# Kernel tuning notes

Hardware: AMD Instinct MI355X
Metric: run time of the kernel (lower is better)

The kernel has to match this reference:

```python
import jax, jax.numpy as jnp
import numpy as np
from jax import lax

N, T, U, V = 32, 512, 100, 4096
BLANK = 0


def setup_inputs() -> dict:
    key = jax.random.key(0)
    k1, k2, k3, k4, k5 = jax.random.split(key, 5)
    encoder_out = jax.random.normal(k1, (N, T, V), dtype=jnp.float32)
    decoder_out = jax.random.normal(k2, (N, U + 1, V), dtype=jnp.float32)
    targets = jax.random.randint(k3, (N, U), 1, V)            # labels, never blank
    input_lengths = jax.random.randint(k4, (N,), T // 2, T + 1)
    target_lengths = jax.random.randint(k5, (N,), U // 2, U + 1)
    return {
        "encoder_out": encoder_out,
        "decoder_out": decoder_out,
        "targets": targets,
        "input_lengths": input_lengths,
        "target_lengths": target_lengths,
    }


def _logprob_single(enc, dec, y, in_len, tgt_len):
    # enc: (T, V)  dec: (U+1, V)  y: (U,)
    Um = y.shape[0]
    u_idx = jnp.arange(Um)
    # emit[t, u] = enc[t, y[u]] + dec[u, y[u]]  (cost of emitting label u+1 at time t)
    emit = enc[:, y] + dec[u_idx, y][None, :]          # (T, U)
    blank_e = enc[:, BLANK]                            # (T,)
    blank_d = dec[:, BLANK]                            # (U+1,)

    # t = 0 row: alpha[0, u] = sum_{k<u} emit[0, k]
    alpha0 = jnp.concatenate([jnp.zeros((1,), enc.dtype), jnp.cumsum(emit[0])])

    def row_step(alpha_prev, xs):
        be_prev, emit_t = xs
        # blank transition from row t-1 (same u)
        top = alpha_prev + be_prev + blank_d           # (U+1,)

        # label transition within row: alpha[u] = logaddexp(top[u], alpha[u-1] + emit_t[u-1])
        def u_step(carry, x):
            top_u, em = x
            a = jnp.logaddexp(top_u, carry + em)
            return a, a

        _, rest = lax.scan(u_step, top[0], (top[1:], emit_t))
        alpha = jnp.concatenate([top[:1], rest])
        return alpha, alpha

    _, rows = lax.scan(row_step, alpha0, (blank_e[:-1], emit[1:]))
    alphas = jnp.concatenate([alpha0[None, :], rows], axis=0)   # (T, U+1)

    # log p(y|x) = alpha[T-1, U] + enc[T-1, blank] + dec[U, blank] with true lengths
    return alphas[in_len - 1, tgt_len] + enc[in_len - 1, BLANK] + dec[tgt_len, BLANK]


def reference(encoder_out, decoder_out, targets, input_lengths, target_lengths):
    # reduction='none': returns per-utterance log p(y|x), shape (N,)
    return jax.vmap(_logprob_single)(encoder_out, decoder_out, targets,
                                     input_lengths, target_lengths)
```

## Files before the change

### kernel.cpp

```cpp
#include <hip/hip_runtime.h>

#define NB 32
#define TT 512
#define UU 100
#define UM 101
#define VV 4096
#define NEG (-1e30f)
#define PW 16
#define WINB 32
#define NWIN 22
#define DST 720
#define L2E 1.4426950408889634f
#define LN2 0.6931471805599453f

__device__ __forceinline__ float vexp2(float x){ float r; asm("v_exp_f32 %0, %1" : "=v"(r) : "v"(x)); return r; }
__device__ __forceinline__ float vlog2(float x){ float r; asm("v_log_f32 %0, %1" : "=v"(r) : "v"(x)); return r; }

__device__ __forceinline__ float lae2(float a, float b) {
    float m  = fmaxf(a, b);
    float nd = fminf(a, b) - m;
    return m + vlog2(1.0f + vexp2(nd));
}

__global__ __launch_bounds__(256) void build_k(
        const float* __restrict__ enc, const float* __restrict__ dec,
        const int* __restrict__ tgt, const int* __restrict__ ilen,
        const int* __restrict__ tlen, float* __restrict__ st) {
    int w = blockIdx.x, n = blockIdx.y;
    int tid = threadIdx.x;
    __shared__ int   tgtL[UU];
    __shared__ float dvxL[UU];
    if (tid < UU) {
        int y = tgt[n * UU + tid];
        tgtL[tid] = y;
        dvxL[tid] = dec[((size_t)n * UM + tid) * VV + y] * L2E;
    }
    int tin = ilen[n], tg = tlen[n];
    __syncthreads();
    const float* encn = enc + (size_t)n * TT * VV;

    float ev[16];
#pragma unroll
    for (int it = 0; it < 16; ++it) {
        int idx = tid + it * 256;
        int dm = idx >> 7, u = idx & 127;
        int d = w * WINB + 1 + dm;
        int t = d - u;
        bool ok = (u >= 1) & (u <= tg) & (t >= 0) & (t < tin);
        ev[it] = NEG;
        if (ok) ev[it] = encn[(size_t)t * VV + tgtL[u - 1]];
    }
#pragma unroll
    for (int it = 0; it < 16; ++it) {
        int idx = tid + it * 256;
        int dm = idx >> 7, u = idx & 127;
        int d = w * WINB + 1 + dm;
        int t = d - u;
        bool ok = (u >= 1) & (u <= tg) & (t >= 0) & (t < tin);
        int uc = max(u, 1);
        float e = ok ? fmaf(ev[it], L2E, dvxL[uc - 1]) : NEG;
        st[((size_t)n * DST + d) * 128 + u] = e;
    }
}

__global__ __launch_bounds__(256) void dp_k(
        const float* __restrict__ enc, const float* __restrict__ dec,
        const int* __restrict__ ilen, const int* __restrict__ tlen,
        const float* __restrict__ st, float* __restrict__ out) {
    int n = blockIdx.x;
    int tid = threadIdx.x;
    __shared__ float blkL[864];
    const float* encn = enc + (size_t)n * TT * VV;
    for (int i = tid; i < 864; i += 256)
        blkL[i] = (i >= 128 && i < 128 + TT) ? encn[(size_t)(i - 128) * VV] * L2E : NEG;
    __syncthreads();
    if (tid >= 64) return;
    int lane = tid;

    int tin = ilen[n], tg = tlen[n];
    int dend = tin - 1 + tg;
    const float* decn = dec + (size_t)n * UM * VV;
    float bd0 = decn[(size_t)min(2 * lane, UM - 1) * VV] * L2E;
    float bd1 = decn[(size_t)min(2 * lane + 1, UM - 1) * VV] * L2E;
    const float* sp = st + (size_t)n * DST * 128 + 2 * lane;
    int ib0 = 127 - 2 * lane;
    bool cap0 = (2 * lane == tg), cap1 = (2 * lane + 1 == tg);
    bool fx16 = (lane == 16), fx32 = (lane == 32), fx48 = (lane == 48);
    float a0 = (lane == 0) ? 0.0f : NEG;
    float a1 = NEG;
    float res = NEG;

    float Ae0[PW], Ae1[PW], Ab0[PW], Ab1[PW];
    float Be0[PW], Be1[PW], Bb0[PW], Bb1[PW];

    auto REFILL = [&](float (&Re0)[PW], float (&Re1)[PW],
                      float (&Rb0)[PW], float (&Rb1)[PW], int d0) {
#pragma unroll
        for (int k = 0; k < PW; ++k) {
            int d = d0 + k;
            float2 ev = *(const float2*)(sp + (size_t)d * 128);
            Re0[k] = ev.x; Re1[k] = ev.y;
            Rb0[k] = blkL[ib0 + d] + bd0;
            Rb1[k] = blkL[ib0 + d - 1] + bd1;
        }
        __builtin_amdgcn_sched_barrier(0);
    };

    auto STEPS = [&](float (&Re0)[PW], float (&Re1)[PW],
                     float (&Rb0)[PW], float (&Rb1)[PW], int d0) {
#pragma unroll
        for (int k = 0; k < PW; ++k) {
            int dd = d0 + k;
            int sh = __builtin_amdgcn_update_dpp(__float_as_int(NEG), __float_as_int(a1),
                                                 0x111, 0xF, 0xF, false);
            float s15 = __int_as_float(__builtin_amdgcn_readlane(__float_as_int(a1), 15));
            float s31 = __int_as_float(__builtin_amdgcn_readlane(__float_as_int(a1), 31));
            float s47 = __int_as_float(__builtin_amdgcn_readlane(__float_as_int(a1), 47));
            float l0 = __int_as_float(sh);
            l0 = fx16 ? s15 : l0;
            l0 = fx32 ? s31 : l0;
            l0 = fx48 ? s47 : l0;
            float bt0 = a0 + Rb0[k], et0 = l0 + Re0[k];
            float bt1 = a1 + Rb1[k], et1 = a0 + Re1[k];
            a0 = lae2(bt0, et0);
            a1 = lae2(bt1, et1);
            if (dd == dend) { if (cap0) res = a0; if (cap1) res = a1; }
        }
        __builtin_amdgcn_sched_barrier(0);
    };

    REFILL(Ae0, Ae1, Ab0, Ab1, 1);
    for (int d0 = 1; d0 <= dend; d0 += 2 * PW) {
        REFILL(Be0, Be1, Bb0, Bb1, d0 + PW);     STEPS(Ae0, Ae1, Ab0, Ab1, d0);
        REFILL(Ae0, Ae1, Ab0, Ab1, d0 + 2 * PW); STEPS(Be0, Be1, Bb0, Bb1, d0 + PW);
    }

    if (cap0 | cap1) {
        float fin  = blkL[128 + tin - 1];
        float bdtg = decn[(size_t)tg * VV] * L2E;
        out[n] = (res + fin + bdtg) * LN2;
    }
}

extern "C" void kernel_launch(void* const* d_in, const int* in_sizes, int n_in,
                              void* d_out, int out_size, void* d_ws, size_t ws_size,
                              hipStream_t hs) {
    const float* enc  = (const float*)d_in[0];
    const float* dec  = (const float*)d_in[1];
    const int*   tgt  = (const int*)d_in[2];
    const int*   ilen = (const int*)d_in[3];
    const int*   tlen = (const int*)d_in[4];
    float* out = (float*)d_out;
    float* st  = (float*)d_ws;

    hipLaunchKernelGGL(build_k, dim3(NWIN, NB), dim3(256), 0, hs,
                       enc, dec, tgt, ilen, tlen, st);
    hipLaunchKernelGGL(dp_k, dim3(NB), dim3(256), 0, hs,
                       enc, dec, ilen, tlen, st, out);
}
```

Measured before the change: 73.29 us.

## Fuse gather and DP kernels with per-window flags to overlap producer and consumer

Merges the emission-gather kernel and the diagonal DP kernel into one launch. Producer blocks fill diagonal windows and publish per-window ready flags, while the DP blocks spin on those flags before each refill, so the wavefront recurrence can start before the whole staging buffer is written. It also drops windows past each utterance's length and uses fewer producer blocks that loop over windows. The cost is an extra flag-clear launch, spin-wait latency, and relying on producer blocks being scheduled alongside the spinning consumers.

```diff
diff --git a/kernel.cpp b/kernel.cpp
--- a/kernel.cpp
+++ b/kernel.cpp
@@ -8,7 +8,8 @@
 #define NEG (-1e30f)
 #define PW 16
 #define WINB 32
-#define NWIN 22
+#define NWIN 20
+#define GSTRIDE 5
 #define DST 720
 #define L2E 1.4426950408889634f
 #define LN2 0.6931471805599453f
@@ -22,53 +23,68 @@
     return m + vlog2(1.0f + vexp2(nd));
 }
 
-__global__ __launch_bounds__(256) void build_k(
+__global__ void clear_k(int* __restrict__ flags) {
+    flags[threadIdx.x] = 0;
+}
+
+__global__ __launch_bounds__(256, 1) void fused_k(
         const float* __restrict__ enc, const float* __restrict__ dec,
         const int* __restrict__ tgt, const int* __restrict__ ilen,
-        const int* __restrict__ tlen, float* __restrict__ st) {
-    int w = blockIdx.x, n = blockIdx.y;
+        const int* __restrict__ tlen,
+        float* __restrict__ st, int* __restrict__ flags, float* __restrict__ out) {
+    int bid = blockIdx.x;
     int tid = threadIdx.x;
-    __shared__ int   tgtL[UU];
-    __shared__ float dvxL[UU];
-    if (tid < UU) {
-        int y = tgt[n * UU + tid];
-        tgtL[tid] = y;
-        dvxL[tid] = dec[((size_t)n * UM + tid) * VV + y] * L2E;
+
+    if (bid >= NB) {
+        int pb = bid - NB;
+        int n = pb / GSTRIDE, g = pb % GSTRIDE;
+        __shared__ int   tgtL[UU];
+        __shared__ float dvxL[UU];
+        if (tid < UU) {
+            int y = tgt[n * UU + tid];
+            tgtL[tid] = y;
+            dvxL[tid] = dec[((size_t)n * UM + tid) * VV + y] * L2E;
+        }
+        int tin = ilen[n], tg = tlen[n];
+        __syncthreads();
+        const float* encn = enc + (size_t)n * TT * VV;
+        int* flg = flags + n * NWIN;
+
+        for (int w = g; w < NWIN; w += GSTRIDE) {
+            if (w * WINB + 1 > tin + tg) break;
+            float ev[16];
+#pragma unroll
+            for (int it = 0; it < 16; ++it) {
+                int idx = tid + it * 256;
+                int dm = idx >> 7, u = idx & 127;
+                int d = w * WINB + 1 + dm;
+                int t = d - u;
+                bool ok = (u >= 1) & (u <= tg) & (t >= 0) & (t < tin);
+                ev[it] = NEG;
+                if (ok) ev[it] = encn[(size_t)t * VV + tgtL[u - 1]];
+            }
+#pragma unroll
+            for (int it = 0; it < 16; ++it) {
+                int idx = tid + it * 256;
+                int dm = idx >> 7, u = idx & 127;
+                int d = w * WINB + 1 + dm;
+                int t = d - u;
+                bool ok = (u >= 1) & (u <= tg) & (t >= 0) & (t < tin);
+                int uc = max(u, 1);
+                float e = ok ? fmaf(ev[it], L2E, dvxL[uc - 1]) : NEG;
+                st[((size_t)n * DST + d) * 128 + u] = e;
+            }
+            __syncthreads();
+            if (tid == 0) {
+                __threadfence();
+                atomicExch(&flg[w], 1);
+            }
+            __syncthreads();
+        }
+        return;
     }
-    int tin = ilen[n], tg = tlen[n];
-    __syncthreads();
-    const float* encn = enc + (size_t)n * TT * VV;
 
-    float ev[16];
-#pragma unroll
-    for (int it = 0; it < 16; ++it) {
-        int idx = tid + it * 256;
-        int dm = idx >> 7, u = idx & 127;
-        int d = w * WINB + 1 + dm;
-        int t = d - u;
-        bool ok = (u >= 1) & (u <= tg) & (t >= 0) & (t < tin);
-        ev[it] = NEG;
-        if (ok) ev[it] = encn[(size_t)t * VV + tgtL[u - 1]];
-    }
-#pragma unroll
-    for (int it = 0; it < 16; ++it) {
-        int idx = tid + it * 256;
-        int dm = idx >> 7, u = idx & 127;
-        int d = w * WINB + 1 + dm;
-        int t = d - u;
-        bool ok = (u >= 1) & (u <= tg) & (t >= 0) & (t < tin);
-        int uc = max(u, 1);
-        float e = ok ? fmaf(ev[it], L2E, dvxL[uc - 1]) : NEG;
-        st[((size_t)n * DST + d) * 128 + u] = e;
-    }
-}
-
-__global__ __launch_bounds__(256) void dp_k(
-        const float* __restrict__ enc, const float* __restrict__ dec,
-        const int* __restrict__ ilen, const int* __restrict__ tlen,
-        const float* __restrict__ st, float* __restrict__ out) {
-    int n = blockIdx.x;
-    int tid = threadIdx.x;
+    int n = bid;
     __shared__ float blkL[864];
     const float* encn = enc + (size_t)n * TT * VV;
     for (int i = tid; i < 864; i += 256)
@@ -79,6 +95,7 @@
 
     int tin = ilen[n], tg = tlen[n];
     int dend = tin - 1 + tg;
+    int wlast = (dend - 1) >> 5;
     const float* decn = dec + (size_t)n * UM * VV;
     float bd0 = decn[(size_t)min(2 * lane, UM - 1) * VV] * L2E;
     float bd1 = decn[(size_t)min(2 * lane + 1, UM - 1) * VV] * L2E;
@@ -89,17 +106,34 @@
     float a0 = (lane == 0) ? 0.0f : NEG;
     float a1 = NEG;
     float res = NEG;
+    int* flg = flags + n * NWIN;
+    int wseen = -1;
 
     float Ae0[PW], Ae1[PW], Ab0[PW], Ab1[PW];
     float Be0[PW], Be1[PW], Bb0[PW], Bb1[PW];
 
+    auto WAITW = [&](int w) {
+        w = min(w, wlast);
+        while (wseen < w) {
+            ++wseen;
+            if (lane == 0) {
+                while (__hip_atomic_load(&flg[wseen], __ATOMIC_ACQUIRE,
+                                         __HIP_MEMORY_SCOPE_AGENT) == 0) {}
+            }
+        }
+    };
+
     auto REFILL = [&](float (&Re0)[PW], float (&Re1)[PW],
                       float (&Rb0)[PW], float (&Rb1)[PW], int d0) {
+        WAITW((d0 + PW - 2) >> 5);
 #pragma unroll
         for (int k = 0; k < PW; ++k) {
             int d = d0 + k;
-            float2 ev = *(const float2*)(sp + (size_t)d * 128);
-            Re0[k] = ev.x; Re1[k] = ev.y;
+            unsigned long long raw = __hip_atomic_load(
+                (const unsigned long long*)(sp + (size_t)d * 128),
+                __ATOMIC_RELAXED, __HIP_MEMORY_SCOPE_AGENT);
+            union { unsigned long long q; float2 f; } cv; cv.q = raw;
+            Re0[k] = cv.f.x; Re1[k] = cv.f.y;
             Rb0[k] = blkL[ib0 + d] + bd0;
             Rb1[k] = blkL[ib0 + d - 1] + bd1;
         }
@@ -151,10 +185,11 @@
     const int*   ilen = (const int*)d_in[3];
     const int*   tlen = (const int*)d_in[4];
     float* out = (float*)d_out;
-    float* st  = (float*)d_ws;
 
-    hipLaunchKernelGGL(build_k, dim3(NWIN, NB), dim3(256), 0, hs,
-                       enc, dec, tgt, ilen, tlen, st);
-    hipLaunchKernelGGL(dp_k, dim3(NB), dim3(256), 0, hs,
-                       enc, dec, ilen, tlen, st, out);
+    float* st    = (float*)d_ws;
+    int*   flags = (int*)(st + (size_t)NB * DST * 128);
+
+    hipLaunchKernelGGL(clear_k, dim3(1), dim3(NB * NWIN), 0, hs, flags);
+    hipLaunchKernelGGL(fused_k, dim3(NB + NB * GSTRIDE), dim3(256), 0, hs,
+                       enc, dec, tgt, ilen, tlen, st, flags, out);
 }
```

After: 81.06 us. 10.6% more time.
